# Kernel optimization log

Hardware: AMD Instinct MI355X
Metric: run time of the kernel (lower is better)

The kernel has to match this reference:

```python
import jax, jax.numpy as jnp
import numpy as np

# ---- Cl(3,0,1) projective geometric algebra tables (GATr basis ordering) ----
_BASIS = [(), (0,), (1,), (2,), (3,),
          (0, 1), (0, 2), (0, 3), (1, 2), (1, 3), (2, 3),
          (0, 1, 2), (0, 1, 3), (0, 2, 3), (1, 2, 3), (0, 1, 2, 3)]
_IDX = {b: i for i, b in enumerate(_BASIS)}
_METRIC = (0.0, 1.0, 1.0, 1.0)  # e0^2 = 0, e1^2 = e2^2 = e3^2 = 1


def _blade_product(a, b):
    arr = list(a) + list(b)
    sign = 1.0
    for i in range(len(arr)):
        for j in range(len(arr) - 1):
            if arr[j] > arr[j + 1]:
                arr[j], arr[j + 1] = arr[j + 1], arr[j]
                sign = -sign
    out, i = [], 0
    while i < len(arr):
        if i + 1 < len(arr) and arr[i] == arr[i + 1]:
            sign *= _METRIC[arr[i]]
            i += 2
        else:
            out.append(arr[i])
            i += 1
    return sign, tuple(out)


def _build_cayley():
    c = np.zeros((16, 16, 16), np.float32)
    for i, a in enumerate(_BASIS):
        for j, b in enumerate(_BASIS):
            s, blade = _blade_product(a, b)
            if s != 0.0:
                c[i, j, _IDX[blade]] += s
    return c

_CAYLEY = _build_cayley()                      # (16,16,16) geometric-product table
_DUAL_FLIP = np.arange(15, -1, -1)             # index reversal permutation
_DUAL_SIGNS = np.array([_blade_product(_BASIS[15 - j], _BASIS[j])[0] for j in range(16)], np.float32)


def _embed_point(p):
    # GATr-style PGA point embedding into trivector components: mv dim 16
    mv = jnp.zeros(p.shape[:-1] + (16,), p.dtype)
    mv = mv.at[..., 14].set(1.0)          # e123 (homogeneous coord)
    mv = mv.at[..., 13].set(p[..., 0])    # e023 <- x
    mv = mv.at[..., 12].set(-p[..., 1])   # e013 <- -y
    mv = mv.at[..., 11].set(p[..., 2])    # e012 <- z
    return mv


def _nn_gather(query, points):
    # brute-force K=1 NN: for each query point return its nearest neighbor in `points`
    # squared distances (B,N,M) via ||q||^2 + ||p||^2 - 2 q.p
    d = (jnp.sum(query * query, -1)[..., :, None]
         + jnp.sum(points * points, -1)[..., None, :]
         - 2.0 * jnp.einsum('bnd,bmd->bnm', query, points))
    idx = jnp.argmin(d, axis=-1)  # (B,N) int32
    return jnp.take_along_axis(points, idx[..., None], axis=1)  # (B,N,3)


def _geometric_product_loss(pred, tgt):
    cayley = jnp.asarray(_CAYLEY, pred.dtype)
    gp = jnp.einsum('ijk,...i,...j->...k', cayley, pred, tgt)  # (B,N,16)
    diff = pred - tgt
    dual = jnp.asarray(_DUAL_SIGNS, diff.dtype) * diff[..., _DUAL_FLIP]
    loss = jnp.mean(jnp.linalg.norm(gp, axis=-1) + jnp.linalg.norm(dual, axis=-1))
    # normalize to [0,1] with min_loss=1.0, max_loss=3.0
    return jnp.clip((loss - 1.0) / 2.0, 0.0, 1.0)


def setup_inputs() -> dict:
    key = jax.random.key(0)
    k1, k2 = jax.random.split(key)
    B, N = 2, 8192
    return {
        'source_points': jax.random.normal(k1, (B, N, 3), jnp.float32),
        'target_points': jax.random.normal(k2, (B, N, 3), jnp.float32),
    }


def reference(source_points, target_points):
    # source -> nearest target, target -> nearest source
    new_target_points = _nn_gather(source_points, target_points)  # (B,N,3)
    new_source_points = _nn_gather(target_points, source_points)  # (B,N,3)

    mv_source = _embed_point(source_points)
    mv_target = _embed_point(target_points)
    mv_new_source = _embed_point(new_source_points)
    mv_new_target = _embed_point(new_target_points)

    gp_loss_t2s = _geometric_product_loss(mv_source, mv_new_target)
    gp_loss_s2t = _geometric_product_loss(mv_new_source, mv_target)
    return 0.5 * (gp_loss_t2s + gp_loss_s2t)
```

## Files before the change

kernel.cpp:

```cpp
#include <hip/hip_runtime.h>


typedef short short8 __attribute__((ext_vector_type(8)));
typedef float f32x16 __attribute__((ext_vector_type(16)));

#define PPB      1024
#define PS       8
#define LDS_HALF 576
#define LDS_TILE 1152


__device__ __forceinline__ unsigned short bf16h(float f) {
    unsigned u = __float_as_uint(f);
    return (unsigned short)((u + 0x7fffu + ((u >> 16) & 1u)) >> 16);
}
__device__ __forceinline__ float bf16v(unsigned short h) {
    return __uint_as_float((unsigned)h << 16);
}

__global__ __launch_bounds__(256, 4)
void nn_kernel(const float* __restrict__ src, const float* __restrict__ tgt,
               float* __restrict__ partial, double* __restrict__ acc,
               unsigned* __restrict__ counter, int N) {
    __shared__ __align__(16) unsigned char Alds[32 * LDS_TILE];

    const int t = threadIdx.x;
    if (blockIdx.x == 0) {
        if (t < 2) acc[t] = 0.0;
        if (t == 2) *counter = 0u;
    }

    const int l   = t & 63, w = t >> 6;
    const int nqc = N >> 8;
    const int bpt = nqc * PS;
    const int task = blockIdx.x / bpt;
    const int rem  = blockIdx.x % bpt;
    const int qc = rem / PS, pc = rem % PS;

    const int pcloud = task ^ 2;
    const float* pRaw = (pcloud < 2 ? src : tgt)
                        + (size_t)3 * ((size_t)(pcloud & 1) * N + (size_t)pc * PPB);
    #pragma unroll
    for (int k = 0; k < 4; ++k) {
        const int j = t + k * 256;
        const float x = pRaw[3*j], y = pRaw[3*j+1], z = pRaw[3*j+2];
        const float pp = x*x + y*y + z*z;
        unsigned short A16[16];
        const float p3[3] = {x, y, z};
        #pragma unroll
        for (int d = 0; d < 3; ++d) {
            const float m2 = -2.0f * p3[d];
            const unsigned short th = bf16h(m2);
            A16[d] = th; A16[4+d] = th; A16[8+d] = bf16h(m2 - bf16v(th));
        }
        const unsigned short pph = bf16h(pp);
        A16[3] = pph; A16[7] = bf16h(pp - bf16v(pph)); A16[11] = 0;
        A16[12] = A16[13] = A16[14] = A16[15] = 0;
        const int tile = j >> 5, r = j & 31;
        unsigned char* base = Alds + tile * LDS_TILE + r * 16 + (r >> 3) * 16;
        *(short8*)(base)            = *(const short8*)(A16);
        *(short8*)(base + LDS_HALF) = *(const short8*)(A16 + 8);
    }

    const int col = l & 31, h = l >> 5;
    const float* qRaw = (task < 2 ? src : tgt)
                        + (size_t)3 * (size_t)((task & 1) * N);
    const int qloc = qc * 256 + w * 64 + col;
    float qa[3], qb[3];
    #pragma unroll
    for (int d = 0; d < 3; ++d) {
        qa[d] = qRaw[3*qloc + d];
        qb[d] = qRaw[3*(qloc+32) + d];
    }
    const float qqa = qa[0]*qa[0] + qa[1]*qa[1] + qa[2]*qa[2];
    const float qqb = qb[0]*qb[0] + qb[1]*qb[1] + qb[2]*qb[2];

    unsigned short B0[8], B1[8];
    #pragma unroll
    for (int d = 0; d < 3; ++d) {
        const unsigned short ha = bf16h(qa[d]);
        const unsigned short hb = bf16h(qb[d]);
        B0[d] = ha; B1[d] = hb;
        B0[4+d] = (h == 0) ? bf16h(qa[d] - bf16v(ha)) : (unsigned short)0;
        B1[4+d] = (h == 0) ? bf16h(qb[d] - bf16v(hb)) : (unsigned short)0;
    }
    B0[3] = B0[7] = (h == 0) ? (unsigned short)0x3F80 : (unsigned short)0;
    B1[3] = B1[7] = B0[3];
    const short8 b0 = *(const short8*)B0;
    const short8 b1 = *(const short8*)B1;

    __syncthreads();

    const int lbase = h * LDS_HALF + col * 16 + (col >> 3) * 16;
    float best0 = 3.4e38f, best1 = 3.4e38f;
    const f32x16 zero = {};
    #pragma unroll 4
    for (int i = 0; i < 32; ++i) {
        const short8 a = *(const short8*)(Alds + i * LDS_TILE + lbase);
        f32x16 d0 = __builtin_amdgcn_mfma_f32_32x32x16_bf16(a, b0, zero, 0, 0, 0);
        f32x16 d1 = __builtin_amdgcn_mfma_f32_32x32x16_bf16(a, b1, zero, 0, 0, 0);
        best0 = fminf(fminf(d0[0],  d0[1]),  best0);
        best0 = fminf(fminf(d0[2],  d0[3]),  best0);
        best0 = fminf(fminf(d0[4],  d0[5]),  best0);
        best0 = fminf(fminf(d0[6],  d0[7]),  best0);
        best0 = fminf(fminf(d0[8],  d0[9]),  best0);
        best0 = fminf(fminf(d0[10], d0[11]), best0);
        best0 = fminf(fminf(d0[12], d0[13]), best0);
        best0 = fminf(fminf(d0[14], d0[15]), best0);
        best1 = fminf(fminf(d1[0],  d1[1]),  best1);
        best1 = fminf(fminf(d1[2],  d1[3]),  best1);
        best1 = fminf(fminf(d1[4],  d1[5]),  best1);
        best1 = fminf(fminf(d1[6],  d1[7]),  best1);
        best1 = fminf(fminf(d1[8],  d1[9]),  best1);
        best1 = fminf(fminf(d1[10], d1[11]), best1);
        best1 = fminf(fminf(d1[12], d1[13]), best1);
        best1 = fminf(fminf(d1[14], d1[15]), best1);
    }

    best0 = fminf(best0, __shfl_xor(best0, 32));
    best1 = fminf(best1, __shfl_xor(best1, 32));
    if (l < 32) {
        const int q0 = task * N + qc * 256 + w * 64 + l;
        float* dst = partial + (size_t)pc * (size_t)(4 * N);
        dst[q0]      = fmaxf(best0 + qqa, 0.0f);
        dst[q0 + 32] = fmaxf(best1 + qqb, 0.0f);
    }
}

__global__ __launch_bounds__(256)
void reduce_kernel(const float* __restrict__ partial, double* __restrict__ acc,
                   unsigned* __restrict__ counter, float* __restrict__ out, int N) {
    const int gq = blockIdx.x * 256 + threadIdx.x;
    const int QT = 4 * N;
    float d2 = partial[gq];
    #pragma unroll
    for (int ps = 1; ps < PS; ++ps)
        d2 = fminf(d2, partial[(size_t)ps * QT + gq]);
    float f = sqrtf(1.0f + d2) + sqrtf(d2);
    for (int o = 32; o > 0; o >>= 1) f += __shfl_down(f, o);
    const int dir = gq / (2 * N);
    if ((threadIdx.x & 63) == 0) atomicAdd(&acc[dir], (double)f);
    __syncthreads();
    if (threadIdx.x == 0) {
        __threadfence();
        const unsigned old = atomicAdd(counter, 1u);
        if (old == gridDim.x - 1) {
            const double s0 = atomicAdd(&acc[0], 0.0);
            const double s1 = atomicAdd(&acc[1], 0.0);
            const double inv = 1.0 / (double)(2 * N);
            double l0 = (s0 * inv - 1.0) * 0.5;
            double l1 = (s1 * inv - 1.0) * 0.5;
            l0 = l0 < 0.0 ? 0.0 : (l0 > 1.0 ? 1.0 : l0);
            l1 = l1 < 0.0 ? 0.0 : (l1 > 1.0 ? 1.0 : l1);
            out[0] = (float)(0.5 * (l0 + l1));
        }
    }
}

extern "C" void kernel_launch(void* const* d_in, const int* in_sizes, int n_in,
                              void* d_out, int out_size, void* d_ws, size_t ws_size,
                              hipStream_t stream) {
    const float* src = (const float*)d_in[0];
    const float* tgt = (const float*)d_in[1];
    float* out = (float*)d_out;

    const int twoN = in_sizes[0] / 3;
    const int N    = twoN / 2;
    const int QT   = 4 * N;

    unsigned* counter = (unsigned*)d_ws;
    double* acc       = (double*)((char*)d_ws + 16);
    float* partial    = (float*)((char*)d_ws + 64);

    const int blocks = 4 * (N >> 8) * (N / PPB);
    nn_kernel<<<blocks, 256, 0, stream>>>(src, tgt, partial, acc, counter, N);

    reduce_kernel<<<QT / 256, 256, 0, stream>>>(partial, acc, counter, out, N);
}
```

Baseline: 26.21 us.

## Fuse NN search and reduction into one kernel using atomicMin and last-block detection

Merges the reduce kernel into the NN kernel. Per-query minimum distances are combined with atomicMin on float bits instead of being written to a partial buffer. The last chunk block for each query group computes that group's loss sum, and the last of those finalises the output. A memset to 0x7f initialises the minima, counters and accumulators. This removes a kernel launch and the partial-buffer round trip, at the cost of an extra memset op and contended atomics.

```diff
diff --git a/kernel.cpp b/kernel.cpp
--- a/kernel.cpp
+++ b/kernel.cpp
@@ -19,17 +19,13 @@
 }
 
 __global__ __launch_bounds__(256, 4)
-void nn_kernel(const float* __restrict__ src, const float* __restrict__ tgt,
-               float* __restrict__ partial, double* __restrict__ acc,
-               unsigned* __restrict__ counter, int N) {
+void fused_kernel(const float* __restrict__ src, const float* __restrict__ tgt,
+                  unsigned* __restrict__ chunkCnt, unsigned* __restrict__ finalCnt,
+                  unsigned* __restrict__ accP, unsigned* __restrict__ d2min,
+                  float* __restrict__ out, int N) {
     __shared__ __align__(16) unsigned char Alds[32 * LDS_TILE];
 
-    const int t = threadIdx.x;
-    if (blockIdx.x == 0) {
-        if (t < 2) acc[t] = 0.0;
-        if (t == 2) *counter = 0u;
-    }
-
+    const int t   = threadIdx.x;
     const int l   = t & 63, w = t >> 6;
     const int nqc = N >> 8;
     const int bpt = nqc * PS;
@@ -119,41 +115,56 @@
 
     best0 = fminf(best0, __shfl_xor(best0, 32));
     best1 = fminf(best1, __shfl_xor(best1, 32));
+    const int qbase = task * N + qc * 256;
     if (l < 32) {
-        const int q0 = task * N + qc * 256 + w * 64 + l;
-        float* dst = partial + (size_t)pc * (size_t)(4 * N);
-        dst[q0]      = fmaxf(best0 + qqa, 0.0f);
-        dst[q0 + 32] = fmaxf(best1 + qqb, 0.0f);
+        const int q0 = qbase + w * 64 + l;
+        unsigned o0 = atomicMin(&d2min[q0],
+                                __float_as_uint(fmaxf(best0 + qqa, 0.0f)));
+        unsigned o1 = atomicMin(&d2min[q0 + 32],
+                                __float_as_uint(fmaxf(best1 + qqb, 0.0f)));
+        asm volatile("" :: "v"(o0), "v"(o1));
     }
-}
 
-__global__ __launch_bounds__(256)
-void reduce_kernel(const float* __restrict__ partial, double* __restrict__ acc,
-                   unsigned* __restrict__ counter, float* __restrict__ out, int N) {
-    const int gq = blockIdx.x * 256 + threadIdx.x;
-    const int QT = 4 * N;
-    float d2 = partial[gq];
+    __shared__ int lastChunk;
+    __syncthreads();
+    if (t == 0)
+        lastChunk = (atomicAdd(&chunkCnt[task * nqc + qc], 1u)
+                     == 0x7f7f7f7fu + (unsigned)PS - 1u);
+    __syncthreads();
+    if (!lastChunk) return;
+
+    const float d2 = __uint_as_float(atomicOr(&d2min[qbase + t], 0u));
+    double fv = (double)(sqrtf(1.0f + d2) + sqrtf(d2));
     #pragma unroll
-    for (int ps = 1; ps < PS; ++ps)
-        d2 = fminf(d2, partial[(size_t)ps * QT + gq]);
-    float f = sqrtf(1.0f + d2) + sqrtf(d2);
-    for (int o = 32; o > 0; o >>= 1) f += __shfl_down(f, o);
-    const int dir = gq / (2 * N);
-    if ((threadIdx.x & 63) == 0) atomicAdd(&acc[dir], (double)f);
+    for (int o = 32; o > 0; o >>= 1) fv += __shfl_down(fv, o);
+    __shared__ double wsum[4];
+    __shared__ int lastFinal;
+    if (l == 0) wsum[w] = fv;
     __syncthreads();
-    if (threadIdx.x == 0) {
-        __threadfence();
-        const unsigned old = atomicAdd(counter, 1u);
-        if (old == gridDim.x - 1) {
-            const double s0 = atomicAdd(&acc[0], 0.0);
-            const double s1 = atomicAdd(&acc[1], 0.0);
-            const double inv = 1.0 / (double)(2 * N);
-            double l0 = (s0 * inv - 1.0) * 0.5;
-            double l1 = (s1 * inv - 1.0) * 0.5;
-            l0 = l0 < 0.0 ? 0.0 : (l0 > 1.0 ? 1.0 : l0);
-            l1 = l1 < 0.0 ? 0.0 : (l1 > 1.0 ? 1.0 : l1);
-            out[0] = (float)(0.5 * (l0 + l1));
-        }
+    if (t == 0) {
+        const float csum = (float)(wsum[0] + wsum[1] + wsum[2] + wsum[3]);
+        unsigned oldA = atomicExch(&accP[task * nqc + qc], __float_as_uint(csum));
+        asm volatile("" :: "v"(oldA));
+        lastFinal = (atomicAdd(finalCnt, 1u)
+                     == 0x7f7f7f7fu + (unsigned)(4 * nqc) - 1u);
+    }
+    __syncthreads();
+    if (!lastFinal) return;
+
+    __shared__ float pvals[128];
+    const int ncid = 4 * nqc;
+    if (t < ncid) pvals[t] = __uint_as_float(atomicOr(&accP[t], 0u));
+    __syncthreads();
+    if (t == 0) {
+        double s0 = 0.0, s1 = 0.0;
+        for (int i = 0; i < ncid / 2; ++i)        s0 += (double)pvals[i];
+        for (int i = ncid / 2; i < ncid; ++i)     s1 += (double)pvals[i];
+        const double inv = 1.0 / (double)(2 * N);
+        double l0 = (s0 * inv - 1.0) * 0.5;
+        double l1 = (s1 * inv - 1.0) * 0.5;
+        l0 = l0 < 0.0 ? 0.0 : (l0 > 1.0 ? 1.0 : l0);
+        l1 = l1 < 0.0 ? 0.0 : (l1 > 1.0 ? 1.0 : l1);
+        out[0] = (float)(0.5 * (l0 + l1));
     }
 }
 
@@ -168,12 +179,14 @@
     const int N    = twoN / 2;
     const int QT   = 4 * N;
 
-    unsigned* counter = (unsigned*)d_ws;
-    double* acc       = (double*)((char*)d_ws + 16);
-    float* partial    = (float*)((char*)d_ws + 64);
+    unsigned* chunkCnt = (unsigned*)d_ws;
+    unsigned* finalCnt = (unsigned*)((char*)d_ws + 512);
+    unsigned* accP     = (unsigned*)((char*)d_ws + 1024);
+    unsigned* d2min    = (unsigned*)((char*)d_ws + 2048);
 
-    const int blocks = 4 * (N >> 8) * (N / PPB);
-    nn_kernel<<<blocks, 256, 0, stream>>>(src, tgt, partial, acc, counter, N);
+    hipMemsetAsync(d_ws, 0x7f, 2048 + (size_t)QT * sizeof(unsigned), stream);
 
-    reduce_kernel<<<QT / 256, 256, 0, stream>>>(partial, acc, counter, out, N);
+    const int blocks = 4 * (N >> 8) * PS;
+    fused_kernel<<<blocks, 256, 0, stream>>>(src, tgt, chunkCnt, finalCnt,
+                                             accP, d2min, out, N);
 }
```

Result: faster. 24.78 us (-5.5%).
